# Kernel optimization log

Measured on AMD Instinct MI355X. Metric: run time of the kernel, lower is better.

Reference implementation:

```python
import jax, jax.numpy as jnp
import numpy as np

C = 256   # in_channels
H = 48
W = 48
B = 2     # batch after chunking into 3 frames; input batch = 3*B
F = 3     # frames (torch.chunk(x, 3))
G = 4     # GroupNorm groups
EPS = 1e-6


def setup_inputs() -> dict:
    key = jax.random.key(0)
    ks = jax.random.split(key, 10)
    s = C ** -0.5  # keep q/k magnitudes sane so softmax is not saturated
    return {
        "x":    jax.random.normal(ks[0], (F * B, C, H, W), jnp.float32),
        "gn_w": jnp.ones((C,), jnp.float32),
        "gn_b": jnp.zeros((C,), jnp.float32),
        "wq":   jax.random.normal(ks[1], (C, C), jnp.float32) * s,
        "bq":   jax.random.normal(ks[2], (C,), jnp.float32) * 0.02,
        "wk":   jax.random.normal(ks[3], (C, C), jnp.float32) * s,
        "bk":   jax.random.normal(ks[4], (C,), jnp.float32) * 0.02,
        "wv":   jax.random.normal(ks[5], (C, C), jnp.float32) * s,
        "bv":   jax.random.normal(ks[6], (C,), jnp.float32) * 0.02,
        "wp":   jax.random.normal(ks[7], (C, C), jnp.float32) * s,
        "bp":   jax.random.normal(ks[8], (C,), jnp.float32) * 0.02,
    }


def reference(x, gn_w, gn_b, wq, bq, wk, bk, wv, bv, wp, bp):
    B3, c, h, w = x.shape
    b = B3 // F
    # torch.chunk(x, 3) + stack(dim=2) -> (b, c, f, h, w); chunk index is frame
    hx = jnp.moveaxis(x.reshape(F, b, c, h, w), 0, 2)  # (b, c, f, h, w)

    # GroupNorm(num_groups=4, eps=1e-6, affine)
    hg = hx.reshape(b, G, c // G, F, h, w)
    mu = hg.mean(axis=(2, 3, 4, 5), keepdims=True)
    var = hg.var(axis=(2, 3, 4, 5), keepdims=True)
    hn = ((hg - mu) * jax.lax.rsqrt(var + EPS)).reshape(b, c, F, h, w)
    hn = hn * gn_w[None, :, None, None, None] + gn_b[None, :, None, None, None]

    # 1x1x1 Conv3d == channel matmul over flattened tokens n = (f h w)
    n = F * h * w
    hf = hn.reshape(b, c, n)                                  # (b, c, n)
    q = jnp.einsum('oc,bcn->bon', wq, hf) + bq[None, :, None]
    k = jnp.einsum('oc,bcn->bon', wk, hf) + bk[None, :, None]
    v = jnp.einsum('oc,bcn->bon', wv, hf) + bv[None, :, None]

    # scores[b,n,m] = sum_c q[b,c,n] * k[b,c,m], scaled by c^-0.5, softmax over m
    scores = jnp.einsum('bcn,bcm->bnm', q, k) * (c ** -0.5)
    attn = jax.nn.softmax(scores, axis=-1)                    # (b, n, n)

    # out[b,c,n] = sum_m v[b,c,m] * attn[b,n,m]
    o = jnp.einsum('bcm,bnm->bcn', v, attn)
    o = jnp.einsum('oc,bcn->bon', wp, o) + bp[None, :, None]  # proj_out

    o = o.reshape(b, c, F, h, w)
    # permute(0,2,1,3,4) then merge (b f) -> batch (b-major, f-minor)
    o = jnp.moveaxis(o, 2, 1).reshape(B3, c, h, w)
    return x + o
```

## Files before the change

kernel.cpp:

```cpp
#include <hip/hip_runtime.h>
#include <stdint.h>

#define CDIM 256
#define HW 2304
#define FR 3
#define NBATCH 2
#define NTOK 6912
#define EPSV 1e-6f
#define LOG2E 1.44269504088896f
#define QSCALE (0.0625f * 1.44269504088896f)

typedef __attribute__((ext_vector_type(8))) short short8;
typedef __attribute__((ext_vector_type(4))) float f32x4;
typedef unsigned short u16;

__device__ inline u16 f2bf(float f) {
  union { float f; uint32_t u; } v; v.f = f;
  uint32_t r = v.u + 0x7FFFu + ((v.u >> 16) & 1u);
  return (u16)(r >> 16);
}
__device__ inline float bf2f(u16 h) {
  union { uint32_t u; float f; } v; v.u = ((uint32_t)h) << 16; return v.f;
}
__device__ inline void gload16(const void* g, void* l) {
  __builtin_amdgcn_global_load_lds(
      (const __attribute__((address_space(1))) void*)g,
      (__attribute__((address_space(3))) void*)l, 16, 0, 0);
}

__global__ void cvt_w_k(const float* wq, const float* wk, const float* wv,
                        const float* wp, u16* wb) {
  int idx = blockIdx.x * 256 + threadIdx.x;
  wb[0 * 65536 + idx] = f2bf(wq[idx] * QSCALE);
  wb[1 * 65536 + idx] = f2bf(wk[idx]);
  wb[2 * 65536 + idx] = f2bf(wv[idx]);
  wb[3 * 65536 + idx] = f2bf(wp[idx]);
}

__global__ void gn_part_k(const float* x, float* part) {
  int bg = blockIdx.x >> 5, sl = blockIdx.x & 31;
  int b = bg >> 2, g = bg & 3;
  int tid = threadIdx.x;
  float s1 = 0.f, s2 = 0.f;
  for (int i = tid; i < 2 * NTOK; i += 256) {
    int cl = sl * 2 + (i / NTOK); int rem = i % NTOK;
    int f = rem / HW; int hw = rem - f * HW;
    float v = x[((size_t)(f * NBATCH + b) * CDIM + g * 64 + cl) * HW + hw];
    s1 += v; s2 += v * v;
  }
  #pragma unroll
  for (int m = 32; m >= 1; m >>= 1) {
    s1 += __shfl_xor(s1, m, 64);
    s2 += __shfl_xor(s2, m, 64);
  }
  __shared__ float r1[4], r2[4];
  int wid = tid >> 6;
  if ((tid & 63) == 0) { r1[wid] = s1; r2[wid] = s2; }
  __syncthreads();
  if (tid == 0) {
    part[blockIdx.x * 2 + 0] = r1[0] + r1[1] + r1[2] + r1[3];
    part[blockIdx.x * 2 + 1] = r2[0] + r2[1] + r2[2] + r2[3];
  }
}

__global__ void gn_fin_k(const float* part, float* stats) {
  int tid = threadIdx.x;
  if (tid < 8) {
    float s1 = 0.f, s2 = 0.f;
    for (int s = 0; s < 32; ++s) {
      s1 += part[(tid * 32 + s) * 2 + 0];
      s2 += part[(tid * 32 + s) * 2 + 1];
    }
    float inv = 1.f / (64.f * NTOK);
    float mu = s1 * inv;
    float var = s2 * inv - mu * mu;
    stats[tid * 2 + 0] = mu;
    stats[tid * 2 + 1] = rsqrtf(var + EPSV);
  }
}

__global__ void gn_apply_k(const float* x, const float* gn_w, const float* gn_b,
                           const float* stats, u16* hn) {
  int nt = blockIdx.x, ct = blockIdx.y, b = blockIdx.z;
  int tid = threadIdx.x;
  __shared__ float tile[64][65];
  int n0 = nt * 64; int f = n0 / HW; int hw0 = n0 - f * HW;
  float mu = stats[(b * 4 + ct) * 2 + 0];
  float rs = stats[(b * 4 + ct) * 2 + 1];
  #pragma unroll
  for (int i = 0; i < 16; ++i) {
    int lin = i * 256 + tid;
    int cr = lin >> 6, nc = lin & 63;
    int c = ct * 64 + cr;
    float v = x[((size_t)(f * NBATCH + b) * CDIM + c) * HW + hw0 + nc];
    tile[cr][nc] = (v - mu) * rs * gn_w[c] + gn_b[c];
  }
  __syncthreads();
  #pragma unroll
  for (int i = 0; i < 16; ++i) {
    int lin = i * 256 + tid;
    int nr = lin >> 6, cc = lin & 63;
    hn[((size_t)b * NTOK + n0 + nr) * CDIM + ct * 64 + cc] = f2bf(tile[cc][nr]);
  }
}

__global__ __launch_bounds__(256) void qkv_k(const u16* hn, const u16* wb,
    const float* bq, const float* bk, const float* bv,
    u16* qb, u16* kb, u16* vb) {
  int nt = blockIdx.x;
  int op = blockIdx.y >> 1, b = blockIdx.y & 1;
  int tid = threadIdx.x, lane = tid & 63, wid = tid >> 6;
  int lr = lane & 15, lg = lane >> 4;
  __shared__ __align__(16) char hn_lds[32768];
  {
    const char* src = (const char*)(hn + ((size_t)b * NTOK + nt * 64) * CDIM);
    #pragma unroll
    for (int i = 0; i < 8; ++i) {
      int off = i * 4096 + wid * 1024 + lane * 16;
      int row = off >> 9;
      gload16(src + (off ^ ((row & 7) << 4)), hn_lds + i * 4096 + wid * 1024);
    }
  }
  __syncthreads();
  f32x4 acc[16];
  #pragma unroll
  for (int i = 0; i < 16; ++i) acc[i] = (f32x4){0.f, 0.f, 0.f, 0.f};
  const u16* wsrc = wb + op * 65536;
  __builtin_amdgcn_s_setprio(1);
  #pragma unroll
  for (int cc = 0; cc < 4; ++cc) {
    short8 afr[2];
    #pragma unroll
    for (int kc = 0; kc < 2; ++kc) {
      int row = wid * 16 + lr;
      int byte = row * 512 + (cc * 64 + kc * 32 + lg * 8) * 2;
      afr[kc] = *(const short8*)(hn_lds + (byte ^ ((row & 7) << 4)));
    }
    #pragma unroll
    for (int cot = 0; cot < 16; ++cot) {
      #pragma unroll
      for (int kc = 0; kc < 2; ++kc) {
        short8 bfr = *(const short8*)(wsrc + (size_t)(cot * 16 + lr) * CDIM +
                                      cc * 64 + kc * 32 + lg * 8);
        acc[cot] = __builtin_amdgcn_mfma_f32_16x16x32_bf16(afr[kc], bfr, acc[cot], 0, 0, 0);
      }
    }
  }
  __builtin_amdgcn_s_setprio(0);
  const float* bias = (op == 0) ? bq : (op == 1) ? bk : bv;
  float bscale = (op == 0) ? QSCALE : 1.0f;
  int nbase = nt * 64 + wid * 16 + lg * 4;
  #pragma unroll
  for (int cot = 0; cot < 16; ++cot) {
    int co = cot * 16 + lr;
    float bv_ = bias[co] * bscale;
    #pragma unroll
    for (int j = 0; j < 4; ++j) {
      float val = acc[cot][j] + bv_;
      int n = nbase + j;
      if (op == 2) {
        int tile = n >> 6, m = n & 63;
        int slot = ((m >> 3) + co) & 7;
        vb[(size_t)b * NTOK * CDIM + (size_t)tile * 16384 + co * 64 +
           slot * 8 + (m & 7)] = f2bf(val);
      } else if (op == 1) {
        int tile = n >> 6, row = n & 63;
        int slot = ((co >> 3) + 2 * row) & 31;
        kb[(size_t)b * NTOK * CDIM + (size_t)tile * 16384 + row * 256 +
           slot * 8 + (co & 7)] = f2bf(val);
      } else {
        qb[((size_t)b * NTOK + n) * CDIM + co] = f2bf(val);
      }
    }
  }
}

template <int TPB, bool SPLIT>
__global__ __launch_bounds__(512, 2) void flash_k(const u16* qb, const u16* kb,
                                                  const u16* vb, u16* opart,
                                                  float* ml, u16* ob) {
  int qt = blockIdx.x, b = blockIdx.y, sp = blockIdx.z;
  int tid = threadIdx.x, lane = tid & 63, wid = tid >> 6;
  int lr = lane & 15, lg = lane >> 4;
  __shared__ __align__(16) char k_lds[2][32768];
  __shared__ __align__(16) char v_lds[2][32768];
  __shared__ __align__(16) char p_lds[8][2048];

  short8 aq[8];
  int nq = qt * 128 + wid * 16 + lr;
  const u16* qsrc = qb + ((size_t)b * NTOK + nq) * CDIM;
  #pragma unroll
  for (int kc = 0; kc < 8; ++kc) aq[kc] = *(const short8*)(qsrc + kc * 32 + lg * 8);

  float mrun = -1e30f, lrun = 0.f;
  f32x4 acc[16];
  #pragma unroll
  for (int i = 0; i < 16; ++i) acc[i] = (f32x4){0.f, 0.f, 0.f, 0.f};

  const char* kbb = (const char*)(kb + (size_t)b * NTOK * CDIM);
  const char* vbb = (const char*)(vb + (size_t)b * NTOK * CDIM);
  char* pw = p_lds[wid];

  {
    const char* ks = kbb + (size_t)(sp * TPB) * 32768;
    const char* vs = vbb + (size_t)(sp * TPB) * 32768;
    #pragma unroll
    for (int i = 0; i < 4; ++i) {
      gload16(ks + wid * 4096 + i * 1024 + lane * 16,
              k_lds[0] + wid * 4096 + i * 1024);
      gload16(vs + wid * 4096 + i * 1024 + lane * 16,
              v_lds[0] + wid * 4096 + i * 1024);
    }
  }
  __syncthreads();

  for (int t = 0; t < TPB; ++t) {
    int cur = t & 1;
    int kt = sp * TPB + t;
    if (t + 1 < TPB) {
      const char* ks = kbb + (size_t)(kt + 1) * 32768;
      const char* vs = vbb + (size_t)(kt + 1) * 32768;
      #pragma unroll
      for (int i = 0; i < 4; ++i) {
        gload16(ks + wid * 4096 + i * 1024 + lane * 16,
                k_lds[cur ^ 1] + wid * 4096 + i * 1024);
        gload16(vs + wid * 4096 + i * 1024 + lane * 16,
                v_lds[cur ^ 1] + wid * 4096 + i * 1024);
      }
    }
    f32x4 s[4];
    __builtin_amdgcn_s_setprio(1);
    #pragma unroll
    for (int mt = 0; mt < 4; ++mt) {
      f32x4 a = (f32x4){0.f, 0.f, 0.f, 0.f};
      #pragma unroll
      for (int kc = 0; kc < 8; ++kc) {
        int row = mt * 16 + lr;
        int slot = (kc * 4 + lg + 2 * row) & 31;
        short8 kf = *(const short8*)(k_lds[cur] + row * 512 + slot * 16);
        a = __builtin_amdgcn_mfma_f32_16x16x32_bf16(kf, aq[kc], a, 0, 0, 0);
      }
      s[mt] = a;
    }
    __builtin_amdgcn_s_setprio(0);
    float m0 = fmaxf(fmaxf(s[0][0], s[0][1]), fmaxf(s[0][2], s[0][3]));
    float m1 = fmaxf(fmaxf(s[1][0], s[1][1]), fmaxf(s[1][2], s[1][3]));
    float m2 = fmaxf(fmaxf(s[2][0], s[2][1]), fmaxf(s[2][2], s[2][3]));
    float m3 = fmaxf(fmaxf(s[3][0], s[3][1]), fmaxf(s[3][2], s[3][3]));
    float pmax = fmaxf(fmaxf(m0, m1), fmaxf(m2, m3));
    pmax = fmaxf(pmax, __shfl_xor(pmax, 16, 64));
    pmax = fmaxf(pmax, __shfl_xor(pmax, 32, 64));
    float mn = mrun;
    if (__any(pmax > mrun + 6.0f)) {
      mn = fmaxf(mrun, pmax);
      float r = exp2f(mrun - mn);
      mrun = mn;
      lrun *= r;
      #pragma unroll
      for (int i = 0; i < 16; ++i) {
        acc[i][0] *= r; acc[i][1] *= r; acc[i][2] *= r; acc[i][3] *= r;
      }
    }
    float ls = 0.f;
    #pragma unroll
    for (int mt = 0; mt < 4; ++mt) {
      #pragma unroll
      for (int j = 0; j < 4; ++j) {
        float p = exp2f(s[mt][j] - mn);
        s[mt][j] = p;
        ls += p;
      }
    }
    ls += __shfl_xor(ls, 16, 64);
    ls += __shfl_xor(ls, 32, 64);
    lrun += ls;
    #pragma unroll
    for (int mt = 0; mt < 4; ++mt) {
      #pragma unroll
      for (int tp = 0; tp < 2; ++tp) {
        uint32_t pk = (uint32_t)f2bf(s[mt][2 * tp]) |
                      ((uint32_t)f2bf(s[mt][2 * tp + 1]) << 16);
        int byte = lr * 128 + mt * 32 + lg * 8 + tp * 4;
        *(uint32_t*)(pw + (byte ^ ((lr & 7) << 4))) = pk;
      }
    }
    __builtin_amdgcn_s_setprio(1);
    #pragma unroll
    for (int mc = 0; mc < 2; ++mc) {
      int pb = lr * 128 + mc * 64 + lg * 16;
      short8 bfr = *(const short8*)(pw + (pb ^ ((lr & 7) << 4)));
      #pragma unroll
      for (int ct = 0; ct < 16; ++ct) {
        int row = ct * 16 + lr;
        int slot = (mc * 4 + lg + row) & 7;
        short8 av = *(const short8*)(v_lds[cur] + row * 128 + slot * 16);
        acc[ct] = __builtin_amdgcn_mfma_f32_16x16x32_bf16(av, bfr, acc[ct], 0, 0, 0);
      }
    }
    __builtin_amdgcn_s_setprio(0);
    __syncthreads();
  }

  int n = qt * 128 + wid * 16 + lr;
  if (!SPLIT) {
    float linv = 1.0f / lrun;
    #pragma unroll
    for (int ct = 0; ct < 16; ++ct) {
      #pragma unroll
      for (int j = 0; j < 4; ++j) {
        int c = ct * 16 + lg * 4 + j;
        ob[((size_t)b * NTOK + n) * CDIM + c] = f2bf(acc[ct][j] * linv);
      }
    }
  } else {
    size_t pbase = (size_t)(sp * 2 + b) * CDIM * NTOK;
    #pragma unroll
    for (int ct = 0; ct < 16; ++ct) {
      #pragma unroll
      for (int j = 0; j < 4; ++j) {
        int c = ct * 16 + lg * 4 + j;
        opart[pbase + (size_t)c * NTOK + n] = f2bf(acc[ct][j]);
      }
    }
    if (lg == 0) {
      ml[((size_t)(sp * 2 + b) * 2 + 0) * NTOK + n] = mrun;
      ml[((size_t)(sp * 2 + b) * 2 + 1) * NTOK + n] = lrun;
    }
  }
}

__global__ __launch_bounds__(256) void comb_k(const u16* opart, const float* ml,
                                              u16* ob) {
  int nt = blockIdx.x, b = blockIdx.y;
  int tid = threadIdx.x;
  int n = nt * 64 + (tid & 63);
  int cchunk = tid >> 6;
  float m0 = ml[((size_t)(0 * 2 + b) * 2 + 0) * NTOK + n];
  float l0 = ml[((size_t)(0 * 2 + b) * 2 + 1) * NTOK + n];
  float m1 = ml[((size_t)(1 * 2 + b) * 2 + 0) * NTOK + n];
  float l1 = ml[((size_t)(1 * 2 + b) * 2 + 1) * NTOK + n];
  float M = fmaxf(m0, m1);
  float w0 = exp2f(m0 - M), w1 = exp2f(m1 - M);
  float inv = 1.f / (w0 * l0 + w1 * l1);
  float a0 = w0 * inv, a1 = w1 * inv;
  const u16* p0 = opart + (size_t)(0 * 2 + b) * CDIM * NTOK;
  const u16* p1 = opart + (size_t)(1 * 2 + b) * CDIM * NTOK;
  u16 buf[64];
  #pragma unroll
  for (int i = 0; i < 64; ++i) {
    int c = cchunk * 64 + i;
    float v = a0 * bf2f(p0[(size_t)c * NTOK + n]) +
              a1 * bf2f(p1[(size_t)c * NTOK + n]);
    buf[i] = f2bf(v);
  }
  #pragma unroll
  for (int i = 0; i < 8; ++i)
    *(short8*)(ob + ((size_t)b * NTOK + n) * CDIM + cchunk * 64 + i * 8) =
        *(const short8*)(buf + i * 8);
}

__global__ __launch_bounds__(256) void proj_k(const u16* ob, const u16* wb,
    const float* bp, const float* x, float* out) {
  int nt = blockIdx.x, b = blockIdx.y, z = blockIdx.z;
  int tid = threadIdx.x, lane = tid & 63, wid = tid >> 6;
  int lr = lane & 15, lg = lane >> 4;
  __shared__ __align__(16) char o_lds[32768];
  const u16* wpb = wb + 3 * 65536;
  {
    const char* src = (const char*)(ob + ((size_t)b * NTOK + nt * 64) * CDIM);
    #pragma unroll
    for (int i = 0; i < 8; ++i) {
      int off = i * 4096 + wid * 1024 + lane * 16;
      int row = off >> 9;
      gload16(src + (off ^ ((row & 7) << 4)), o_lds + i * 4096 + wid * 1024);
    }
  }
  __syncthreads();
  #pragma unroll
  for (int ct2 = 0; ct2 < 2; ++ct2) {
    int cot = z * 8 + wid * 2 + ct2;
    short8 aw[8];
    #pragma unroll
    for (int kc = 0; kc < 8; ++kc)
      aw[kc] = *(const short8*)(wpb + (size_t)(cot * 16 + lr) * CDIM + kc * 32 + lg * 8);
    #pragma unroll
    for (int ntile = 0; ntile < 4; ++ntile) {
      f32x4 a = (f32x4){0.f, 0.f, 0.f, 0.f};
      #pragma unroll
      for (int kc = 0; kc < 8; ++kc) {
        int row = ntile * 16 + lr;
        int byte = row * 512 + (kc * 32 + lg * 8) * 2;
        short8 bfr = *(const short8*)(o_lds + (byte ^ ((row & 7) << 4)));
        a = __builtin_amdgcn_mfma_f32_16x16x32_bf16(aw[kc], bfr, a, 0, 0, 0);
      }
      int n = nt * 64 + ntile * 16 + lr;
      int f = n / HW; int hw = n - f * HW;
      #pragma unroll
      for (int j = 0; j < 4; ++j) {
        int co = cot * 16 + lg * 4 + j;
        float val = a[j] + bp[co];
        size_t oi = ((size_t)(b * FR + f) * CDIM + co) * HW + hw;
        out[oi] = x[oi] + val;
      }
    }
  }
}

extern "C" void kernel_launch(void* const* d_in, const int* in_sizes, int n_in,
                              void* d_out, int out_size, void* d_ws, size_t ws_size,
                              hipStream_t stream) {
  const float* x    = (const float*)d_in[0];
  const float* gn_w = (const float*)d_in[1];
  const float* gn_b = (const float*)d_in[2];
  const float* wq   = (const float*)d_in[3];
  const float* bq   = (const float*)d_in[4];
  const float* wk   = (const float*)d_in[5];
  const float* bk   = (const float*)d_in[6];
  const float* wv   = (const float*)d_in[7];
  const float* bv   = (const float*)d_in[8];
  const float* wp   = (const float*)d_in[9];
  const float* bp   = (const float*)d_in[10];
  float* out = (float*)d_out;
  char* ws = (char*)d_ws;

  float* stats = (float*)(ws + 0);
  float* part  = (float*)(ws + 256);
  u16* wb = (u16*)(ws + 4096);
  u16* hn = (u16*)(ws + 528384);
  u16* qb = (u16*)(ws + 7606272);
  u16* kb = (u16*)(ws + 14684160);
  u16* vb = (u16*)(ws + 21762048);
  u16* ob = (u16*)(ws + 28839936);
  u16* opart = (u16*)(ws + 35917824);
  float* ml  = (float*)(ws + 50073600);
  const size_t NEED_SPLIT = 50294784;

  cvt_w_k<<<256, 256, 0, stream>>>(wq, wk, wv, wp, wb);
  gn_part_k<<<256, 256, 0, stream>>>(x, part);
  gn_fin_k<<<1, 64, 0, stream>>>(part, stats);
  gn_apply_k<<<dim3(108, 4, 2), 256, 0, stream>>>(x, gn_w, gn_b, stats, hn);
  qkv_k<<<dim3(108, 6), 256, 0, stream>>>(hn, wb, bq, bk, bv, qb, kb, vb);
  if (ws_size >= NEED_SPLIT) {
    flash_k<54, true><<<dim3(54, 2, 2), 512, 0, stream>>>(qb, kb, vb, opart, ml, ob);
    comb_k<<<dim3(108, 2), 256, 0, stream>>>(opart, ml, ob);
  } else {
    flash_k<108, false><<<dim3(54, 2, 1), 512, 0, stream>>>(qb, kb, vb, opart, ml, ob);
  }
  proj_k<<<dim3(108, 2, 2), 256, 0, stream>>>(ob, wb, bp, x, out);
}
```

Before: 267.8 us.

## Double query rows per flash wave, split KV four ways, vectorize stores

Each flash wave now handles two 16-row query groups against every K/V tile it loads into LDS, so each tile is reused for 256 queries per block instead of 128. The KV range is split four ways instead of two, which keeps the grid at 216 blocks. The partial output layout becomes token-major so flash and combine can use vector stores and loads, and the combine kernel merges four partials. The QKV epilogue swaps MFMA operand order for q/k so it can write packed 4-element stores, and the weight-conversion kernel is merged into the GroupNorm partial-sum launch. The cost is double the accumulator registers per wave, which raises spill and occupancy risk under launch_bounds(512,2), plus a larger workspace requirement.

```diff
diff --git a/kernel.cpp b/kernel.cpp
--- a/kernel.cpp
+++ b/kernel.cpp
@@ -7,10 +7,10 @@
 #define NBATCH 2
 #define NTOK 6912
 #define EPSV 1e-6f
-#define LOG2E 1.44269504088896f
 #define QSCALE (0.0625f * 1.44269504088896f)
 
 typedef __attribute__((ext_vector_type(8))) short short8;
+typedef __attribute__((ext_vector_type(4))) short short4v;
 typedef __attribute__((ext_vector_type(4))) float f32x4;
 typedef unsigned short u16;
 
@@ -28,16 +28,17 @@
       (__attribute__((address_space(3))) void*)l, 16, 0, 0);
 }
 
-__global__ void cvt_w_k(const float* wq, const float* wk, const float* wv,
-                        const float* wp, u16* wb) {
-  int idx = blockIdx.x * 256 + threadIdx.x;
-  wb[0 * 65536 + idx] = f2bf(wq[idx] * QSCALE);
-  wb[1 * 65536 + idx] = f2bf(wk[idx]);
-  wb[2 * 65536 + idx] = f2bf(wv[idx]);
-  wb[3 * 65536 + idx] = f2bf(wp[idx]);
-}
-
-__global__ void gn_part_k(const float* x, float* part) {
+__global__ void pre_k(const float* x, float* part, const float* wq,
+                      const float* wk, const float* wv, const float* wp,
+                      u16* wb) {
+  if (blockIdx.x >= 256) {
+    int idx = (blockIdx.x - 256) * 256 + threadIdx.x;
+    wb[0 * 65536 + idx] = f2bf(wq[idx] * QSCALE);
+    wb[1 * 65536 + idx] = f2bf(wk[idx]);
+    wb[2 * 65536 + idx] = f2bf(wv[idx]);
+    wb[3 * 65536 + idx] = f2bf(wp[idx]);
+    return;
+  }
   int bg = blockIdx.x >> 5, sl = blockIdx.x & 31;
   int b = bg >> 2, g = bg & 3;
   int tid = threadIdx.x;
@@ -142,40 +143,51 @@
       for (int kc = 0; kc < 2; ++kc) {
         short8 bfr = *(const short8*)(wsrc + (size_t)(cot * 16 + lr) * CDIM +
                                       cc * 64 + kc * 32 + lg * 8);
-        acc[cot] = __builtin_amdgcn_mfma_f32_16x16x32_bf16(afr[kc], bfr, acc[cot], 0, 0, 0);
+        if (op == 2)
+          acc[cot] = __builtin_amdgcn_mfma_f32_16x16x32_bf16(afr[kc], bfr, acc[cot], 0, 0, 0);
+        else
+          acc[cot] = __builtin_amdgcn_mfma_f32_16x16x32_bf16(bfr, afr[kc], acc[cot], 0, 0, 0);
       }
     }
   }
   __builtin_amdgcn_s_setprio(0);
-  const float* bias = (op == 0) ? bq : (op == 1) ? bk : bv;
-  float bscale = (op == 0) ? QSCALE : 1.0f;
-  int nbase = nt * 64 + wid * 16 + lg * 4;
-  #pragma unroll
-  for (int cot = 0; cot < 16; ++cot) {
-    int co = cot * 16 + lr;
-    float bv_ = bias[co] * bscale;
-    #pragma unroll
-    for (int j = 0; j < 4; ++j) {
-      float val = acc[cot][j] + bv_;
-      int n = nbase + j;
-      if (op == 2) {
-        int tile = n >> 6, m = n & 63;
-        int slot = ((m >> 3) + co) & 7;
-        vb[(size_t)b * NTOK * CDIM + (size_t)tile * 16384 + co * 64 +
-           slot * 8 + (m & 7)] = f2bf(val);
-      } else if (op == 1) {
-        int tile = n >> 6, row = n & 63;
+  if (op == 2) {
+    int m0 = wid * 16 + lg * 4;
+    char* vtile = (char*)vb + (size_t)b * NTOK * CDIM * 2 + (size_t)nt * 32768;
+    #pragma unroll
+    for (int cot = 0; cot < 16; ++cot) {
+      int co = cot * 16 + lr;
+      float bb = bv[co];
+      short4v r;
+      #pragma unroll
+      for (int j = 0; j < 4; ++j) r[j] = (short)f2bf(acc[cot][j] + bb);
+      int slot = ((m0 >> 3) + co) & 7;
+      *(short4v*)(vtile + co * 128 + slot * 16 + (m0 & 7) * 2) = r;
+    }
+  } else {
+    int row = wid * 16 + lr;
+    int n = nt * 64 + row;
+    const float* bias = (op == 0) ? bq : bk;
+    float bscale = (op == 0) ? QSCALE : 1.0f;
+    char* ktile = (char*)kb + (size_t)b * NTOK * CDIM * 2 + (size_t)nt * 32768;
+    #pragma unroll
+    for (int cot = 0; cot < 16; ++cot) {
+      int co = cot * 16 + lg * 4;
+      f32x4 b4 = *(const f32x4*)(bias + co);
+      short4v r;
+      #pragma unroll
+      for (int j = 0; j < 4; ++j) r[j] = (short)f2bf(acc[cot][j] + b4[j] * bscale);
+      if (op == 0) {
+        *(short4v*)(qb + ((size_t)b * NTOK + n) * CDIM + co) = r;
+      } else {
         int slot = ((co >> 3) + 2 * row) & 31;
-        kb[(size_t)b * NTOK * CDIM + (size_t)tile * 16384 + row * 256 +
-           slot * 8 + (co & 7)] = f2bf(val);
-      } else {
-        qb[((size_t)b * NTOK + n) * CDIM + co] = f2bf(val);
-      }
-    }
-  }
-}
-
-template <int TPB, bool SPLIT>
+        *(short4v*)(ktile + row * 512 + slot * 16 + (co & 7) * 2) = r;
+      }
+    }
+  }
+}
+
+template <bool SPLIT>
 __global__ __launch_bounds__(512, 2) void flash_k(const u16* qb, const u16* kb,
                                                   const u16* vb, u16* opart,
                                                   float* ml, u16* ob) {
@@ -186,24 +198,34 @@
   __shared__ __align__(16) char v_lds[2][32768];
   __shared__ __align__(16) char p_lds[8][2048];
 
-  short8 aq[8];
-  int nq = qt * 128 + wid * 16 + lr;
-  const u16* qsrc = qb + ((size_t)b * NTOK + nq) * CDIM;
-  #pragma unroll
-  for (int kc = 0; kc < 8; ++kc) aq[kc] = *(const short8*)(qsrc + kc * 32 + lg * 8);
-
-  float mrun = -1e30f, lrun = 0.f;
-  f32x4 acc[16];
-  #pragma unroll
-  for (int i = 0; i < 16; ++i) acc[i] = (f32x4){0.f, 0.f, 0.f, 0.f};
+  int t0 = SPLIT ? 27 * sp : 0;
+  int t1 = SPLIT ? 27 * sp + 27 : 108;
+
+  short8 aq0[8], aq1[8];
+  int nq0 = qt * 256 + wid * 32 + lr;
+  const u16* qs0 = qb + ((size_t)b * NTOK + nq0) * CDIM;
+  #pragma unroll
+  for (int kc = 0; kc < 8; ++kc) {
+    aq0[kc] = *(const short8*)(qs0 + kc * 32 + lg * 8);
+    aq1[kc] = *(const short8*)(qs0 + 16 * CDIM + kc * 32 + lg * 8);
+  }
+
+  float mrun0 = -1e30f, lrun0 = 0.f;
+  float mrun1 = -1e30f, lrun1 = 0.f;
+  f32x4 acc0[16], acc1[16];
+  #pragma unroll
+  for (int i = 0; i < 16; ++i) {
+    acc0[i] = (f32x4){0.f, 0.f, 0.f, 0.f};
+    acc1[i] = (f32x4){0.f, 0.f, 0.f, 0.f};
+  }
 
   const char* kbb = (const char*)(kb + (size_t)b * NTOK * CDIM);
   const char* vbb = (const char*)(vb + (size_t)b * NTOK * CDIM);
   char* pw = p_lds[wid];
 
   {
-    const char* ks = kbb + (size_t)(sp * TPB) * 32768;
-    const char* vs = vbb + (size_t)(sp * TPB) * 32768;
+    const char* ks = kbb + (size_t)t0 * 32768;
+    const char* vs = vbb + (size_t)t0 * 32768;
     #pragma unroll
     for (int i = 0; i < 4; ++i) {
       gload16(ks + wid * 4096 + i * 1024 + lane * 16,
@@ -214,12 +236,11 @@
   }
   __syncthreads();
 
-  for (int t = 0; t < TPB; ++t) {
-    int cur = t & 1;
-    int kt = sp * TPB + t;
-    if (t + 1 < TPB) {
-      const char* ks = kbb + (size_t)(kt + 1) * 32768;
-      const char* vs = vbb + (size_t)(kt + 1) * 32768;
+  for (int t = t0; t < t1; ++t) {
+    int cur = (t - t0) & 1;
+    if (t + 1 < t1) {
+      const char* ks = kbb + (size_t)(t + 1) * 32768;
+      const char* vs = vbb + (size_t)(t + 1) * 32768;
       #pragma unroll
       for (int i = 0; i < 4; ++i) {
         gload16(ks + wid * 4096 + i * 1024 + lane * 16,
@@ -228,103 +249,148 @@
                 v_lds[cur ^ 1] + wid * 4096 + i * 1024);
       }
     }
-    f32x4 s[4];
+    f32x4 s0[4], s1[4];
     __builtin_amdgcn_s_setprio(1);
     #pragma unroll
     for (int mt = 0; mt < 4; ++mt) {
-      f32x4 a = (f32x4){0.f, 0.f, 0.f, 0.f};
+      f32x4 a0 = (f32x4){0.f, 0.f, 0.f, 0.f};
+      f32x4 a1 = (f32x4){0.f, 0.f, 0.f, 0.f};
       #pragma unroll
       for (int kc = 0; kc < 8; ++kc) {
         int row = mt * 16 + lr;
         int slot = (kc * 4 + lg + 2 * row) & 31;
         short8 kf = *(const short8*)(k_lds[cur] + row * 512 + slot * 16);
-        a = __builtin_amdgcn_mfma_f32_16x16x32_bf16(kf, aq[kc], a, 0, 0, 0);
-      }
-      s[mt] = a;
+        a0 = __builtin_amdgcn_mfma_f32_16x16x32_bf16(kf, aq0[kc], a0, 0, 0, 0);
+        a1 = __builtin_amdgcn_mfma_f32_16x16x32_bf16(kf, aq1[kc], a1, 0, 0, 0);
+      }
+      s0[mt] = a0; s1[mt] = a1;
     }
     __builtin_amdgcn_s_setprio(0);
-    float m0 = fmaxf(fmaxf(s[0][0], s[0][1]), fmaxf(s[0][2], s[0][3]));
-    float m1 = fmaxf(fmaxf(s[1][0], s[1][1]), fmaxf(s[1][2], s[1][3]));
-    float m2 = fmaxf(fmaxf(s[2][0], s[2][1]), fmaxf(s[2][2], s[2][3]));
-    float m3 = fmaxf(fmaxf(s[3][0], s[3][1]), fmaxf(s[3][2], s[3][3]));
-    float pmax = fmaxf(fmaxf(m0, m1), fmaxf(m2, m3));
-    pmax = fmaxf(pmax, __shfl_xor(pmax, 16, 64));
-    pmax = fmaxf(pmax, __shfl_xor(pmax, 32, 64));
-    float mn = mrun;
-    if (__any(pmax > mrun + 6.0f)) {
-      mn = fmaxf(mrun, pmax);
-      float r = exp2f(mrun - mn);
-      mrun = mn;
-      lrun *= r;
-      #pragma unroll
-      for (int i = 0; i < 16; ++i) {
-        acc[i][0] *= r; acc[i][1] *= r; acc[i][2] *= r; acc[i][3] *= r;
-      }
-    }
-    float ls = 0.f;
-    #pragma unroll
-    for (int mt = 0; mt < 4; ++mt) {
-      #pragma unroll
-      for (int j = 0; j < 4; ++j) {
-        float p = exp2f(s[mt][j] - mn);
-        s[mt][j] = p;
-        ls += p;
-      }
-    }
-    ls += __shfl_xor(ls, 16, 64);
-    ls += __shfl_xor(ls, 32, 64);
-    lrun += ls;
-    #pragma unroll
-    for (int mt = 0; mt < 4; ++mt) {
-      #pragma unroll
-      for (int tp = 0; tp < 2; ++tp) {
-        uint32_t pk = (uint32_t)f2bf(s[mt][2 * tp]) |
-                      ((uint32_t)f2bf(s[mt][2 * tp + 1]) << 16);
-        int byte = lr * 128 + mt * 32 + lg * 8 + tp * 4;
-        *(uint32_t*)(pw + (byte ^ ((lr & 7) << 4))) = pk;
-      }
+    {
+      float px = fmaxf(fmaxf(fmaxf(s0[0][0], s0[0][1]), fmaxf(s0[0][2], s0[0][3])),
+                       fmaxf(fmaxf(s0[1][0], s0[1][1]), fmaxf(s0[1][2], s0[1][3])));
+      px = fmaxf(px, fmaxf(fmaxf(s0[2][0], s0[2][1]), fmaxf(s0[2][2], s0[2][3])));
+      px = fmaxf(px, fmaxf(fmaxf(s0[3][0], s0[3][1]), fmaxf(s0[3][2], s0[3][3])));
+      px = fmaxf(px, __shfl_xor(px, 16, 64));
+      px = fmaxf(px, __shfl_xor(px, 32, 64));
+      if (__any(px > mrun0 + 6.0f)) {
+        float mn = fmaxf(mrun0, px);
+        float r = exp2f(mrun0 - mn);
+        mrun0 = mn; lrun0 *= r;
+        #pragma unroll
+        for (int i = 0; i < 16; ++i) {
+          acc0[i][0] *= r; acc0[i][1] *= r; acc0[i][2] *= r; acc0[i][3] *= r;
+        }
+      }
+      float ls = 0.f;
+      #pragma unroll
+      for (int mt = 0; mt < 4; ++mt) {
+        #pragma unroll
+        for (int j = 0; j < 4; ++j) {
+          float p = exp2f(s0[mt][j] - mrun0);
+          s0[mt][j] = p; ls += p;
+        }
+      }
+      ls += __shfl_xor(ls, 16, 64);
+      ls += __shfl_xor(ls, 32, 64);
+      lrun0 += ls;
+    }
+    {
+      float px = fmaxf(fmaxf(fmaxf(s1[0][0], s1[0][1]), fmaxf(s1[0][2], s1[0][3])),
+                       fmaxf(fmaxf(s1[1][0], s1[1][1]), fmaxf(s1[1][2], s1[1][3])));
+      px = fmaxf(px, fmaxf(fmaxf(s1[2][0], s1[2][1]), fmaxf(s1[2][2], s1[2][3])));
+      px = fmaxf(px, fmaxf(fmaxf(s1[3][0], s1[3][1]), fmaxf(s1[3][2], s1[3][3])));
+      px = fmaxf(px, __shfl_xor(px, 16, 64));
+      px = fmaxf(px, __shfl_xor(px, 32, 64));
+      if (__any(px > mrun1 + 6.0f)) {
+        float mn = fmaxf(mrun1, px);
+        float r = exp2f(mrun1 - mn);
+        mrun1 = mn; lrun1 *= r;
+        #pragma unroll
+        for (int i = 0; i < 16; ++i) {
+          acc1[i][0] *= r; acc1[i][1] *= r; acc1[i][2] *= r; acc1[i][3] *= r;
+        }
+      }
+      float ls = 0.f;
+      #pragma unroll
+      for (int mt = 0; mt < 4; ++mt) {
+        #pragma unroll
+        for (int j = 0; j < 4; ++j) {
+          float p = exp2f(s1[mt][j] - mrun1);
+          s1[mt][j] = p; ls += p;
+        }
+      }
+      ls += __shfl_xor(ls, 16, 64);
+      ls += __shfl_xor(ls, 32, 64);
+      lrun1 += ls;
     }
     __builtin_amdgcn_s_setprio(1);
     #pragma unroll
     for (int mc = 0; mc < 2; ++mc) {
-      int pb = lr * 128 + mc * 64 + lg * 16;
-      short8 bfr = *(const short8*)(pw + (pb ^ ((lr & 7) << 4)));
+      #pragma unroll
+      for (int mt2 = 0; mt2 < 2; ++mt2) {
+        int mt = mc * 2 + mt2;
+        #pragma unroll
+        for (int tp = 0; tp < 2; ++tp) {
+          uint32_t pk0 = (uint32_t)f2bf(s0[mt][2 * tp]) |
+                         ((uint32_t)f2bf(s0[mt][2 * tp + 1]) << 16);
+          uint32_t pk1 = (uint32_t)f2bf(s1[mt][2 * tp]) |
+                         ((uint32_t)f2bf(s1[mt][2 * tp + 1]) << 16);
+          int byte = lr * 128 + (mt2 * 16 + lg * 4 + tp * 2) * 2;
+          *(uint32_t*)(pw + ((byte + 0) ^ ((lr & 7) << 4))) = pk0;
+          *(uint32_t*)(pw + ((byte + 64) ^ ((lr & 7) << 4))) = pk1;
+        }
+      }
+      short8 pf0 = *(const short8*)(pw + ((lr * 128 + lg * 16) ^ ((lr & 7) << 4)));
+      short8 pf1 = *(const short8*)(pw + ((lr * 128 + 64 + lg * 16) ^ ((lr & 7) << 4)));
       #pragma unroll
       for (int ct = 0; ct < 16; ++ct) {
         int row = ct * 16 + lr;
         int slot = (mc * 4 + lg + row) & 7;
         short8 av = *(const short8*)(v_lds[cur] + row * 128 + slot * 16);
-        acc[ct] = __builtin_amdgcn_mfma_f32_16x16x32_bf16(av, bfr, acc[ct], 0, 0, 0);
+        acc0[ct] = __builtin_amdgcn_mfma_f32_16x16x32_bf16(av, pf0, acc0[ct], 0, 0, 0);
+        acc1[ct] = __builtin_amdgcn_mfma_f32_16x16x32_bf16(av, pf1, acc1[ct], 0, 0, 0);
       }
     }
     __builtin_amdgcn_s_setprio(0);
     __syncthreads();
   }
 
-  int n = qt * 128 + wid * 16 + lr;
   if (!SPLIT) {
-    float linv = 1.0f / lrun;
+    float li0 = 1.0f / lrun0, li1 = 1.0f / lrun1;
+    u16* d0 = ob + ((size_t)b * NTOK + nq0) * CDIM;
+    u16* d1 = d0 + 16 * CDIM;
     #pragma unroll
     for (int ct = 0; ct < 16; ++ct) {
+      short4v r0, r1;
       #pragma unroll
       for (int j = 0; j < 4; ++j) {
-        int c = ct * 16 + lg * 4 + j;
-        ob[((size_t)b * NTOK + n) * CDIM + c] = f2bf(acc[ct][j] * linv);
-      }
+        r0[j] = (short)f2bf(acc0[ct][j] * li0);
+        r1[j] = (short)f2bf(acc1[ct][j] * li1);
+      }
+      *(short4v*)(d0 + ct * 16 + lg * 4) = r0;
+      *(short4v*)(d1 + ct * 16 + lg * 4) = r1;
     }
   } else {
-    size_t pbase = (size_t)(sp * 2 + b) * CDIM * NTOK;
+    u16* d0 = opart + ((size_t)(sp * 2 + b) * NTOK + nq0) * CDIM;
+    u16* d1 = d0 + 16 * CDIM;
     #pragma unroll
     for (int ct = 0; ct < 16; ++ct) {
+      short4v r0, r1;
       #pragma unroll
       for (int j = 0; j < 4; ++j) {
-        int c = ct * 16 + lg * 4 + j;
-        opart[pbase + (size_t)c * NTOK + n] = f2bf(acc[ct][j]);
-      }
+        r0[j] = (short)f2bf(acc0[ct][j]);
+        r1[j] = (short)f2bf(acc1[ct][j]);
+      }
+      *(short4v*)(d0 + ct * 16 + lg * 4) = r0;
+      *(short4v*)(d1 + ct * 16 + lg * 4) = r1;
     }
     if (lg == 0) {
-      ml[((size_t)(sp * 2 + b) * 2 + 0) * NTOK + n] = mrun;
-      ml[((size_t)(sp * 2 + b) * 2 + 1) * NTOK + n] = lrun;
+      size_t mb = (size_t)(sp * 2 + b) * 2;
+      ml[(mb + 0) * NTOK + nq0] = mrun0;
+      ml[(mb + 1) * NTOK + nq0] = lrun0;
+      ml[(mb + 0) * NTOK + nq0 + 16] = mrun1;
+      ml[(mb + 1) * NTOK + nq0 + 16] = lrun1;
     }
   }
 }
@@ -333,30 +399,33 @@
                                               u16* ob) {
   int nt = blockIdx.x, b = blockIdx.y;
   int tid = threadIdx.x;
-  int n = nt * 64 + (tid & 63);
-  int cchunk = tid >> 6;
-  float m0 = ml[((size_t)(0 * 2 + b) * 2 + 0) * NTOK + n];
-  float l0 = ml[((size_t)(0 * 2 + b) * 2 + 1) * NTOK + n];
-  float m1 = ml[((size_t)(1 * 2 + b) * 2 + 0) * NTOK + n];
-  float l1 = ml[((size_t)(1 * 2 + b) * 2 + 1) * NTOK + n];
-  float M = fmaxf(m0, m1);
-  float w0 = exp2f(m0 - M), w1 = exp2f(m1 - M);
-  float inv = 1.f / (w0 * l0 + w1 * l1);
-  float a0 = w0 * inv, a1 = w1 * inv;
-  const u16* p0 = opart + (size_t)(0 * 2 + b) * CDIM * NTOK;
-  const u16* p1 = opart + (size_t)(1 * 2 + b) * CDIM * NTOK;
-  u16 buf[64];
-  #pragma unroll
-  for (int i = 0; i < 64; ++i) {
-    int c = cchunk * 64 + i;
-    float v = a0 * bf2f(p0[(size_t)c * NTOK + n]) +
-              a1 * bf2f(p1[(size_t)c * NTOK + n]);
-    buf[i] = f2bf(v);
-  }
-  #pragma unroll
-  for (int i = 0; i < 8; ++i)
-    *(short8*)(ob + ((size_t)b * NTOK + n) * CDIM + cchunk * 64 + i * 8) =
-        *(const short8*)(buf + i * 8);
+  #pragma unroll
+  for (int g = 0; g < 8; ++g) {
+    int n = nt * 64 + g * 8 + (tid >> 5);
+    int c0 = (tid & 31) * 8;
+    float m[4], l[4];
+    #pragma unroll
+    for (int s = 0; s < 4; ++s) {
+      m[s] = ml[((size_t)(s * 2 + b) * 2 + 0) * NTOK + n];
+      l[s] = ml[((size_t)(s * 2 + b) * 2 + 1) * NTOK + n];
+    }
+    float M = fmaxf(fmaxf(m[0], m[1]), fmaxf(m[2], m[3]));
+    float w[4]; float den = 0.f;
+    #pragma unroll
+    for (int s = 0; s < 4; ++s) { w[s] = exp2f(m[s] - M); den += w[s] * l[s]; }
+    float inv = 1.f / den;
+    float o[8] = {0.f, 0.f, 0.f, 0.f, 0.f, 0.f, 0.f, 0.f};
+    #pragma unroll
+    for (int s = 0; s < 4; ++s) {
+      short8 v = *(const short8*)(opart + ((size_t)(s * 2 + b) * NTOK + n) * CDIM + c0);
+      #pragma unroll
+      for (int j = 0; j < 8; ++j) o[j] += w[s] * bf2f((u16)v[j]);
+    }
+    short8 r8;
+    #pragma unroll
+    for (int j = 0; j < 8; ++j) r8[j] = (short)f2bf(o[j] * inv);
+    *(short8*)(ob + ((size_t)b * NTOK + n) * CDIM + c0) = r8;
+  }
 }
 
 __global__ __launch_bounds__(256) void proj_k(const u16* ob, const u16* wb,
@@ -432,19 +501,18 @@
   u16* vb = (u16*)(ws + 21762048);
   u16* ob = (u16*)(ws + 28839936);
   u16* opart = (u16*)(ws + 35917824);
-  float* ml  = (float*)(ws + 50073600);
-  const size_t NEED_SPLIT = 50294784;
-
-  cvt_w_k<<<256, 256, 0, stream>>>(wq, wk, wv, wp, wb);
-  gn_part_k<<<256, 256, 0, stream>>>(x, part);
+  float* ml  = (float*)(ws + 64229376);
+  const size_t NEED_SPLIT = 64671744;
+
+  pre_k<<<512, 256, 0, stream>>>(x, part, wq, wk, wv, wp, wb);
   gn_fin_k<<<1, 64, 0, stream>>>(part, stats);
   gn_apply_k<<<dim3(108, 4, 2), 256, 0, stream>>>(x, gn_w, gn_b, stats, hn);
   qkv_k<<<dim3(108, 6), 256, 0, stream>>>(hn, wb, bq, bk, bv, qb, kb, vb);
   if (ws_size >= NEED_SPLIT) {
-    flash_k<54, true><<<dim3(54, 2, 2), 512, 0, stream>>>(qb, kb, vb, opart, ml, ob);
+    flash_k<true><<<dim3(27, 2, 4), 512, 0, stream>>>(qb, kb, vb, opart, ml, ob);
     comb_k<<<dim3(108, 2), 256, 0, stream>>>(opart, ml, ob);
   } else {
-    flash_k<108, false><<<dim3(54, 2, 1), 512, 0, stream>>>(qb, kb, vb, opart, ml, ob);
+    flash_k<false><<<dim3(27, 2, 1), 512, 0, stream>>>(qb, kb, vb, opart, ml, ob);
   }
   proj_k<<<dim3(108, 2, 2), 256, 0, stream>>>(ob, wb, bp, x, out);
 }
```

New measurement: 274.6 us. +2.5%, slower.
